# Kernel tuning notes

Hardware: AMD Instinct MI355X
Metric: run time of the kernel (lower is better)

Reference implementation:

```python
import jax, jax.numpy as jnp
import numpy as np

NUM_HEADS = 8
QK_CH = 1024
V_CH = 1024
Q_DIM = 1024
KV_DIM = 1024
EPS = 1e-5


def layernorm(x, w, b):
    mu = jnp.mean(x, axis=-1, keepdims=True)
    var = jnp.mean(jnp.square(x - mu), axis=-1, keepdims=True)
    return (x - mu) * jax.lax.rsqrt(var + EPS) * w + b


def setup_inputs() -> dict:
    key = jax.random.key(0)
    ks = jax.random.split(key, 8)
    B, Q, K = 8, 512, 4096
    s = 0.02
    return {
        "hidden_states": jax.random.normal(ks[0], (B, Q, Q_DIM), jnp.float32),
        "inputs": jax.random.normal(ks[1], (B, K, KV_DIM), jnp.float32),
        "ln1_w": jnp.ones((Q_DIM,), jnp.float32),
        "ln1_b": jnp.zeros((Q_DIM,), jnp.float32),
        "ln2_w": jnp.ones((KV_DIM,), jnp.float32),
        "ln2_b": jnp.zeros((KV_DIM,), jnp.float32),
        "Wq": jax.random.normal(ks[2], (QK_CH, Q_DIM), jnp.float32) * s,
        "bq": jnp.zeros((QK_CH,), jnp.float32),
        "Wk": jax.random.normal(ks[3], (QK_CH, KV_DIM), jnp.float32) * s,
        "bk": jnp.zeros((QK_CH,), jnp.float32),
        "Wv": jax.random.normal(ks[4], (V_CH, KV_DIM), jnp.float32) * s,
        "bv": jnp.zeros((V_CH,), jnp.float32),
    }


def reference(hidden_states, inputs, ln1_w, ln1_b, ln2_w, ln2_b, Wq, bq, Wk, bk, Wv, bv):
    B, Qlen, _ = hidden_states.shape
    Klen = inputs.shape[1]
    H = NUM_HEADS
    dqk = QK_CH // H
    dv = V_CH // H

    h = layernorm(hidden_states, ln1_w, ln1_b)
    x = layernorm(inputs, ln2_w, ln2_b)

    # torch Linear: y = x W^T + b
    q = (h @ Wq.T + bq).reshape(B, Qlen, H, dqk).transpose(0, 2, 1, 3)  # b h q d
    k = (x @ Wk.T + bk).reshape(B, Klen, H, dqk).transpose(0, 2, 1, 3)  # b h k d
    v = (x @ Wv.T + bv).reshape(B, Klen, H, dv).transpose(0, 2, 1, 3)   # b h k d

    scores = jnp.einsum("bhqd,bhkd->bhqk", q, k) / jnp.sqrt(jnp.float32(dqk))
    probs = jax.nn.softmax(scores, axis=-1)
    ctx = jnp.einsum("bhqk,bhkd->bhqd", probs, v)
    ctx = ctx.transpose(0, 2, 1, 3).reshape(B, Qlen, H * dv)

    # use_query_residual=True
    return hidden_states + ctx
```

## Files before the change

### kernel.cpp

```cpp
#include <hip/hip_runtime.h>
#include <hip/hip_fp8.h>

typedef __attribute__((ext_vector_type(8))) short short8;
typedef __attribute__((ext_vector_type(4))) short bf16x4;
typedef __attribute__((ext_vector_type(4))) float f32x4;
typedef __attribute__((ext_vector_type(2))) long i64x2;

#define DEV __device__ __forceinline__

DEV unsigned short f2bf(float f) {
    unsigned int u = __builtin_bit_cast(unsigned int, f);
    u += 0x7fffu + ((u >> 16) & 1u);
    return (unsigned short)(u >> 16);
}

DEV unsigned char f2fp8(float f) {
    return __hip_fp8_e4m3(f).__x;
}

#define GLOAD16(gp, lp)                                                        \
    __builtin_amdgcn_global_load_lds(                                          \
        (const __attribute__((address_space(1))) void*)(gp),                   \
        (__attribute__((address_space(3))) void*)(lp), 16, 0, 0)

__global__ __launch_bounds__(256) void prep(
    const float* __restrict__ hidden, const float* __restrict__ inputs,
    const float* __restrict__ ln1w, const float* __restrict__ ln1b,
    const float* __restrict__ ln2w, const float* __restrict__ ln2b,
    const float* __restrict__ Wq, const float* __restrict__ Wk, const float* __restrict__ Wv,
    unsigned char* __restrict__ LNh8, unsigned char* __restrict__ LNx8,
    unsigned char* __restrict__ Wq8, unsigned char* __restrict__ Wk8, unsigned char* __restrict__ Wv8)
{
    if (blockIdx.x < 9216) {
        int row = blockIdx.x * 4 + (threadIdx.x >> 6);
        int lane = threadIdx.x & 63;
        const float *src, *wp, *bp; unsigned char* dst;
        if (row < 4096) { src = hidden + (size_t)row * 1024; wp = ln1w; bp = ln1b; dst = LNh8 + (size_t)row * 1024; }
        else { int r = row - 4096; src = inputs + (size_t)r * 1024; wp = ln2w; bp = ln2b; dst = LNx8 + (size_t)r * 1024; }

        f32x4 v[4];
        float s = 0.f, ss = 0.f;
#pragma unroll
        for (int i = 0; i < 4; ++i) {
            v[i] = *reinterpret_cast<const f32x4*>(src + lane * 16 + i * 4);
#pragma unroll
            for (int j = 0; j < 4; ++j) { s += v[i][j]; ss += v[i][j] * v[i][j]; }
        }
#pragma unroll
        for (int off = 32; off >= 1; off >>= 1) { s += __shfl_xor(s, off); ss += __shfl_xor(ss, off); }
        float mu = s * (1.f / 1024.f);
        float var = fmaxf(ss * (1.f / 1024.f) - mu * mu, 0.f);
        float rs = rsqrtf(var + 1e-5f);

        unsigned char by[16];
#pragma unroll
        for (int i = 0; i < 4; ++i) {
            f32x4 wv = *reinterpret_cast<const f32x4*>(wp + lane * 16 + i * 4);
            f32x4 bv = *reinterpret_cast<const f32x4*>(bp + lane * 16 + i * 4);
#pragma unroll
            for (int j = 0; j < 4; ++j)
                by[i * 4 + j] = f2fp8((v[i][j] - mu) * rs * wv[j] + bv[j]);
        }
        int o = (lane * 16) & 63;
        int s0 = (o < 32) ? 2 * o : 2 * (o - 32) + 8;
        unsigned char* base = dst + (lane >> 2) * 64;
        *reinterpret_cast<unsigned long long*>(base + s0)      = *reinterpret_cast<unsigned long long*>(&by[0]);
        *reinterpret_cast<unsigned long long*>(base + s0 + 16) = *reinterpret_cast<unsigned long long*>(&by[8]);
    } else {
        unsigned tid = (blockIdx.x - 9216) * 256 + threadIdx.x;
        int arr = tid >> 16;
        unsigned idx = tid & 65535u;
        const float* s = (arr == 0) ? Wq : (arr == 1) ? Wk : Wv;
        unsigned char* d = (arr == 0) ? Wq8 : (arr == 1) ? Wk8 : Wv8;
        unsigned char by[16];
#pragma unroll
        for (int i = 0; i < 4; ++i) {
            f32x4 a = *reinterpret_cast<const f32x4*>(s + (size_t)idx * 16 + i * 4);
#pragma unroll
            for (int j = 0; j < 4; ++j) by[i * 4 + j] = f2fp8(a[j] * 64.f);
        }
        int o = (idx & 3) * 16;
        int s0 = (o < 32) ? 2 * o : 2 * (o - 32) + 8;
        unsigned char* base = d + (size_t)(idx >> 2) * 64;
        *reinterpret_cast<unsigned long long*>(base + s0)      = *reinterpret_cast<unsigned long long*>(&by[0]);
        *reinterpret_cast<unsigned long long*>(base + s0 + 16) = *reinterpret_cast<unsigned long long*>(&by[8]);
    }
}

__global__ __launch_bounds__(512, 2) void gemm256(
    const unsigned char* __restrict__ A8, const unsigned char* __restrict__ Ah8,
    const unsigned char* __restrict__ W8, const unsigned char* __restrict__ Wq8,
    const float* __restrict__ bk, const float* __restrict__ bv, const float* __restrict__ bq,
    unsigned short* __restrict__ Cn, unsigned short* __restrict__ Vt, unsigned short* __restrict__ Qm)
{
    __shared__ __align__(16) char smemc[65536];

    int t = threadIdx.x, lane = t & 63, w = t >> 6, g = lane >> 4, lr = lane & 15;
    int wr = w >> 2, wcn = w & 3;
    int R0 = wr * 128, C0 = wcn * 64;

    int id = blockIdx.x;
    int m0, n0, trans = 0;
    const unsigned char *Ab_, *Wb_;
    const float* bias;
    unsigned short* Cout;
    if (id < 1024) {
        int xcd = id & 7, ord = id >> 3;
        int mt = xcd * 16 + ord / 8;
        int nt = ord % 8;
        m0 = mt * 256; n0 = nt * 256;
        Ab_ = A8; Wb_ = W8;
        if (nt < 4) { bias = bk; Cout = Cn; }
        else        { bias = bv; Cout = Vt; trans = 1; }
    } else {
        int id2 = id - 1024;
        int mt = id2 & 15, nt = id2 >> 4;
        m0 = mt * 256; n0 = nt * 256;
        Ab_ = Ah8; Wb_ = Wq8;
        bias = bq; Cout = Qm;
    }

    const unsigned char* Ap = Ab_ + (size_t)m0 * 1024;
    const unsigned char* Wp = Wb_ + (size_t)n0 * 1024;

    f32x4 acc[8][4];
#pragma unroll
    for (int i = 0; i < 8; ++i)
#pragma unroll
        for (int j = 0; j < 4; ++j) acc[i][j] = (f32x4)0.f;

    int schunk = (t & 3) ^ ((t >> 3) & 3);
    auto STAGE1 = [&](int slot, int kt, int q) {
        const unsigned char* P = (q < 2) ? Ap : Wp;
        char* ldsb = smemc + ((q < 2) ? 0 : 32768) + slot * 16384 + (q & 1) * 8192;
        int r = (q & 1) * 128 + (t >> 2);
        const char* gp = (const char*)(P + (size_t)r * 1024 + kt * 64 + schunk * 16);
        GLOAD16(gp, ldsb + (t >> 2) * 64 + (t & 3) * 16);
    };

    STAGE1(0, 0, 0); STAGE1(0, 0, 1); STAGE1(0, 0, 2); STAGE1(0, 0, 3);
    asm volatile("s_waitcnt vmcnt(0)" ::: "memory");
    __builtin_amdgcn_s_barrier();

    int xr = (lr >> 1) & 3;
    int slA = (g ^ xr) * 16;

    for (int kt = 0; kt < 16; ++kt) {
        const int cs = kt & 1;
        const char* Ab = smemc + cs * 16384;
        const char* Bb = smemc + 32768 + cs * 16384;
        i64x2 af[4], bf[4];

#pragma unroll
        for (int a = 0; a < 4; ++a) {
            int r = R0 + a * 16 + lr;
            af[a] = *reinterpret_cast<const i64x2*>(Ab + r * 64 + slA);
        }
#pragma unroll
        for (int ni = 0; ni < 4; ++ni) {
            int r = C0 + ni * 16 + lr;
            bf[ni] = *reinterpret_cast<const i64x2*>(Bb + r * 64 + slA);
        }
        if (kt < 15) { STAGE1(cs ^ 1, kt + 1, 0); STAGE1(cs ^ 1, kt + 1, 1); }
        __builtin_amdgcn_sched_barrier(0);
        __builtin_amdgcn_s_barrier();
        asm volatile("s_waitcnt lgkmcnt(0)" ::: "memory");
        __builtin_amdgcn_sched_barrier(0);
        __builtin_amdgcn_s_setprio(1);
#pragma unroll
        for (int a = 0; a < 4; ++a)
#pragma unroll
            for (int ni = 0; ni < 4; ++ni) {
                acc[a][ni] = __builtin_amdgcn_mfma_f32_16x16x32_fp8_fp8(
                    af[a][0], bf[ni][0], acc[a][ni], 0, 0, 0);
                acc[a][ni] = __builtin_amdgcn_mfma_f32_16x16x32_fp8_fp8(
                    af[a][1], bf[ni][1], acc[a][ni], 0, 0, 0);
            }
        __builtin_amdgcn_s_setprio(0);
        __builtin_amdgcn_sched_barrier(0);
        __builtin_amdgcn_s_barrier();

#pragma unroll
        for (int a = 0; a < 4; ++a) {
            int r = R0 + 64 + a * 16 + lr;
            af[a] = *reinterpret_cast<const i64x2*>(Ab + r * 64 + slA);
        }
        if (kt < 15) { STAGE1(cs ^ 1, kt + 1, 2); STAGE1(cs ^ 1, kt + 1, 3); }
        __builtin_amdgcn_sched_barrier(0);
        __builtin_amdgcn_s_barrier();
        asm volatile("s_waitcnt lgkmcnt(0)" ::: "memory");
        __builtin_amdgcn_sched_barrier(0);
        __builtin_amdgcn_s_setprio(1);
#pragma unroll
        for (int a = 0; a < 4; ++a)
#pragma unroll
            for (int ni = 0; ni < 4; ++ni) {
                acc[4 + a][ni] = __builtin_amdgcn_mfma_f32_16x16x32_fp8_fp8(
                    af[a][0], bf[ni][0], acc[4 + a][ni], 0, 0, 0);
                acc[4 + a][ni] = __builtin_amdgcn_mfma_f32_16x16x32_fp8_fp8(
                    af[a][1], bf[ni][1], acc[4 + a][ni], 0, 0, 0);
            }
        __builtin_amdgcn_s_setprio(0);
        asm volatile("s_waitcnt vmcnt(0)" ::: "memory");
        __builtin_amdgcn_sched_barrier(0);
        __builtin_amdgcn_s_barrier();
    }
    __syncthreads();

    const float SC = 0.015625f;
    unsigned short* CtS = (unsigned short*)smemc;
    if (!trans) {
#pragma unroll
        for (int ch = 0; ch < 4; ++ch) {
            if (ch) __syncthreads();
            if (wr == (ch >> 1)) {
                int ma = (ch & 1) * 4;
#pragma unroll
                for (int ni = 0; ni < 4; ++ni) {
                    int c = C0 + ni * 16 + lr;
                    float bvv = bias[n0 + c];
#pragma unroll
                    for (int a = 0; a < 4; ++a)
#pragma unroll
                        for (int j = 0; j < 4; ++j)
                            CtS[(a * 16 + g * 4 + j) * 272 + c] = f2bf(acc[ma + a][ni][j] * SC + bvv);
                }
            }
            __syncthreads();
#pragma unroll
            for (int it = 0; it < 4; ++it) {
                int u2 = it * 512 + t;
                int row = u2 >> 5, c16 = u2 & 31;
                *reinterpret_cast<short8*>(Cout + (size_t)(m0 + ch * 64 + row) * 1024 + n0 + c16 * 8) =
                    *reinterpret_cast<const short8*>(&CtS[row * 272 + c16 * 8]);
            }
        }
    } else {
        int nt = n0 >> 8;
        int hbase = (nt - 4) * 2;
        int b = m0 >> 12, kv0 = m0 & 4095;
#pragma unroll
        for (int ch = 0; ch < 4; ++ch) {
            if (ch) __syncthreads();
            if (wcn == ch) {
#pragma unroll
                for (int ni = 0; ni < 4; ++ni) {
                    int dl = ni * 16 + lr;
                    float bvv = bias[(nt - 4) * 256 + ch * 64 + dl];
#pragma unroll
                    for (int mi = 0; mi < 8; ++mi)
#pragma unroll
                        for (int j = 0; j < 4; ++j)
                            CtS[dl * 272 + R0 + mi * 16 + g * 4 + j] = f2bf(acc[mi][ni][j] * SC + bvv);
                }
            }
            __syncthreads();
            int hh = hbase + (ch >> 1), dbase = (ch & 1) * 64;
            unsigned short* dst = Cout + ((size_t)(b * 8 + hh) * 128 + dbase) * 4096 + kv0;
#pragma unroll
            for (int it = 0; it < 4; ++it) {
                int u2 = it * 512 + t;
                int row = u2 >> 5, c8 = u2 & 31;
                *reinterpret_cast<short8*>(dst + (size_t)row * 4096 + c8 * 8) =
                    *reinterpret_cast<const short8*>(&CtS[row * 272 + c8 * 8]);
            }
        }
    }
}

__global__ __launch_bounds__(256, 2) void attn_kernel(
    const unsigned short* __restrict__ Qm, const unsigned short* __restrict__ Km,
    const unsigned short* __restrict__ VtG, const float* __restrict__ hidden,
    float* __restrict__ out)
{
    __shared__ __align__(16) unsigned short Kl[2][64 * 128];
    __shared__ __align__(16) unsigned short Vt[2][128 * 64];
    __shared__ __align__(16) unsigned short Pl[64 * 64];

    int t = threadIdx.x, lane = t & 63, w = t >> 6, g = lane >> 4, lr = lane & 15;
    int id = blockIdx.x;
    int swz = (id & 7) * 64 + (id >> 3);
    int qt = swz & 7, h = (swz >> 3) & 7, b = swz >> 6;

    short8 qf[4];
#pragma unroll
    for (int kk = 0; kk < 4; ++kk)
        qf[kk] = *reinterpret_cast<const short8*>(
            Qm + (size_t)(b * 512 + qt * 64 + w * 16 + lr) * 1024 + h * 128 + kk * 32 + g * 8);
    asm volatile("s_waitcnt vmcnt(0)" ::: "memory");

    float m2 = 0.f;
    float l = 0.f;
    f32x4 oacc[8];
#pragma unroll
    for (int nf = 0; nf < 8; ++nf) oacc[nf] = (f32x4)0.f;

    const float SCALE = 0.08838834764831845f;
    const float LOG2E = 1.4426950408889634f;
    const float K1 = SCALE * LOG2E;
    const float THR2 = 11.5f;

    size_t kbase = (size_t)b * 4096 * 1024 + h * 128;
    size_t vbase = ((size_t)(b * 8 + h)) * 128 * 4096;

    auto STAGE_K = [&](int buf, int c) {
        int kv0 = c * 64;
#pragma unroll
        for (int i = 0; i < 4; ++i) {
            int rb = w * 16 + i * 4;
            int row = rb + (lane >> 4);
            int cb = ((lane & 15) * 16) ^ ((row & 7) << 4);
            const char* gp = (const char*)(Km + kbase + (size_t)(kv0 + row) * 1024) + cb;
            GLOAD16(gp, &Kl[buf][rb * 128]);
        }
    };
    auto STAGE_V = [&](int buf, int c) {
        int kv0 = c * 64;
#pragma unroll
        for (int i = 0; i < 4; ++i) {
            int db = w * 32 + i * 8;
            int d = db + (lane >> 3);
            int cb = ((lane & 7) * 16) ^ ((d & 7) << 4);
            const char* gp = (const char*)(VtG + vbase + (size_t)d * 4096 + kv0) + cb;
            GLOAD16(gp, &Vt[buf][db * 64]);
        }
    };

    STAGE_K(0, 0); STAGE_V(0, 0);

    for (int c = 0; c < 64; ++c) {
        int cur = c & 1;
        asm volatile("s_waitcnt vmcnt(0) lgkmcnt(0)" ::: "memory");
        __builtin_amdgcn_sched_barrier(0);
        __builtin_amdgcn_s_barrier();
        if (c < 63) { STAGE_K(cur ^ 1, c + 1); STAGE_V(cur ^ 1, c + 1); }

        f32x4 sacc[4];
#pragma unroll
        for (int nf = 0; nf < 4; ++nf) sacc[nf] = (f32x4)0.f;
#pragma unroll
        for (int kk = 0; kk < 4; ++kk) {
            int cb0 = kk * 64 + g * 16;
            short8 kf[4];
#pragma unroll
            for (int nf = 0; nf < 4; ++nf) {
                int row = nf * 16 + lr;
                kf[nf] = *reinterpret_cast<const short8*>(
                    (const char*)&Kl[cur][0] + row * 256 + (cb0 ^ ((row & 7) << 4)));
            }
            __builtin_amdgcn_s_setprio(1);
#pragma unroll
            for (int nf = 0; nf < 4; ++nf)
                sacc[nf] = __builtin_amdgcn_mfma_f32_16x16x32_bf16(kf[nf], qf[kk], sacc[nf], 0, 0, 0);
            __builtin_amdgcn_s_setprio(0);
        }

        float smax = sacc[0][0];
#pragma unroll
        for (int nf = 0; nf < 4; ++nf)
#pragma unroll
            for (int j = 0; j < 4; ++j) smax = fmaxf(smax, sacc[nf][j]);
        float s2max = smax * K1;
        if (!__all(s2max <= m2 + THR2)) {
            float rm = s2max;
            rm = fmaxf(rm, __shfl_xor(rm, 16));
            rm = fmaxf(rm, __shfl_xor(rm, 32));
            float m2n = fmaxf(m2, rm);
            float corr = exp2f(m2 - m2n);
            l *= corr;
            m2 = m2n;
#pragma unroll
            for (int j = 0; j < 4; ++j) {
                float cj = __shfl(corr, g * 4 + j);
#pragma unroll
                for (int nf = 0; nf < 8; ++nf) oacc[nf][j] *= cj;
            }
        }
        int prow = w * 16 + lr;
        int rsw = (lr & 7) << 4;
#pragma unroll
        for (int nf = 0; nf < 4; ++nf) {
            float p0 = exp2f(sacc[nf][0] * K1 - m2);
            float p1 = exp2f(sacc[nf][1] * K1 - m2);
            float p2 = exp2f(sacc[nf][2] * K1 - m2);
            float p3 = exp2f(sacc[nf][3] * K1 - m2);
            l += (p0 + p1) + (p2 + p3);
            bf16x4 pk;
            pk[0] = (short)f2bf(p0); pk[1] = (short)f2bf(p1);
            pk[2] = (short)f2bf(p2); pk[3] = (short)f2bf(p3);
            *reinterpret_cast<bf16x4*>(
                (char*)Pl + prow * 128 + ((nf * 32 + g * 8) ^ rsw)) = pk;
        }
        asm volatile("s_waitcnt lgkmcnt(0)" ::: "memory");
        __builtin_amdgcn_sched_barrier(0);

#pragma unroll
        for (int kp = 0; kp < 2; ++kp) {
            int cb0 = kp * 64 + g * 16;
            short8 pa = *reinterpret_cast<const short8*>(
                (const char*)Pl + prow * 128 + (cb0 ^ rsw));
#pragma unroll
            for (int nf = 0; nf < 8; ++nf) {
                int d = nf * 16 + lr;
                short8 vb = *reinterpret_cast<const short8*>(
                    (const char*)&Vt[cur][0] + d * 128 + (cb0 ^ ((d & 7) << 4)));
                oacc[nf] = __builtin_amdgcn_mfma_f32_16x16x32_bf16(pa, vb, oacc[nf], 0, 0, 0);
            }
        }
    }

    l += __shfl_xor(l, 16);
    l += __shfl_xor(l, 32);
#pragma unroll
    for (int j = 0; j < 4; ++j) {
        float lj = __shfl(l, g * 4 + j);
        float inv = 1.f / lj;
        int q = qt * 64 + w * 16 + g * 4 + j;
        size_t base = (size_t)(b * 512 + q) * 1024 + h * 128;
#pragma unroll
        for (int nf = 0; nf < 8; ++nf) {
            int d = nf * 16 + lr;
            out[base + d] = hidden[base + d] + oacc[nf][j] * inv;
        }
    }
}

extern "C" void kernel_launch(void* const* d_in, const int* in_sizes, int n_in,
                              void* d_out, int out_size, void* d_ws, size_t ws_size,
                              hipStream_t stream) {
    const float* hidden = (const float*)d_in[0];
    const float* inputs = (const float*)d_in[1];
    const float* ln1w   = (const float*)d_in[2];
    const float* ln1b   = (const float*)d_in[3];
    const float* ln2w   = (const float*)d_in[4];
    const float* ln2b   = (const float*)d_in[5];
    const float* Wq     = (const float*)d_in[6];
    const float* bq     = (const float*)d_in[7];
    const float* Wk     = (const float*)d_in[8];
    const float* bk     = (const float*)d_in[9];
    const float* Wv     = (const float*)d_in[10];
    const float* bv     = (const float*)d_in[11];
    float* out = (float*)d_out;
    char* ws = (char*)d_ws;

    unsigned char* LNh8 = (unsigned char*)ws;
    unsigned char* LNx8 = LNh8 + 4194304;
    unsigned char* Wq8  = LNx8 + 33554432;
    unsigned char* Wk8  = Wq8 + 1048576;
    unsigned char* Wv8  = Wk8 + 1048576;
    unsigned short* Qm  = (unsigned short*)(Wv8 + 1048576);
    unsigned short* Km  = Qm + 4194304;
    unsigned short* VtG = Km + 33554432;

    prep<<<dim3(9984), dim3(256), 0, stream>>>(
        hidden, inputs, ln1w, ln1b, ln2w, ln2b, Wq, Wk, Wv, LNh8, LNx8, Wq8, Wk8, Wv8);
    gemm256<<<dim3(1088), dim3(512), 0, stream>>>(
        LNx8, LNh8, Wk8, Wq8, bk, bv, bq, Km, VtG, Qm);
    attn_kernel<<<dim3(512), dim3(256), 0, stream>>>(Qm, Km, VtG, hidden, out);
}
```

Before: 293.9 us.

## Store Q/K/V and attention probabilities in FP8 and use FP8 MFMA in attention

The projection GEMM now writes Q, K and transposed V as FP8 e4m3 instead of bf16, with a permuted column layout matching the fp8 MFMA operand order. The attention kernel stages half-size K/V tiles, computes QK^T and PV with fp8 MFMA, and packs probabilities to fp8 in LDS with new swizzles. The online-softmax rescale threshold is lowered to limit fp8 range issues on probabilities. This halves the intermediate memory traffic and LDS footprint and uses a higher-throughput MFMA, at the cost of precision in the scores and in the probability accumulation.

Measured after the change: 300.4 us. 1.02x slower.

```diff
diff --git a/kernel.cpp b/kernel.cpp
--- a/kernel.cpp
+++ b/kernel.cpp
@@ -22,6 +22,10 @@
     __builtin_amdgcn_global_load_lds(                                          \
         (const __attribute__((address_space(1))) void*)(gp),                   \
         (__attribute__((address_space(3))) void*)(lp), 16, 0, 0)
+
+DEV int pi64(int o) {
+    return (o < 32) ? ((o >> 3) * 16 + (o & 7)) : (((o - 32) >> 3) * 16 + 8 + (o & 7));
+}
 
 __global__ __launch_bounds__(256) void prep(
     const float* __restrict__ hidden, const float* __restrict__ inputs,
@@ -91,7 +95,7 @@
     const unsigned char* __restrict__ A8, const unsigned char* __restrict__ Ah8,
     const unsigned char* __restrict__ W8, const unsigned char* __restrict__ Wq8,
     const float* __restrict__ bk, const float* __restrict__ bv, const float* __restrict__ bq,
-    unsigned short* __restrict__ Cn, unsigned short* __restrict__ Vt, unsigned short* __restrict__ Qm)
+    unsigned char* __restrict__ Cn, unsigned char* __restrict__ Vt, unsigned char* __restrict__ Qm)
 {
     __shared__ __align__(16) char smemc[65536];
 
@@ -103,7 +107,7 @@
     int m0, n0, trans = 0;
     const unsigned char *Ab_, *Wb_;
     const float* bias;
-    unsigned short* Cout;
+    unsigned char* Cout;
     if (id < 1024) {
         int xcd = id & 7, ord = id >> 3;
         int mt = xcd * 16 + ord / 8;
@@ -208,7 +212,7 @@
     __syncthreads();
 
     const float SC = 0.015625f;
-    unsigned short* CtS = (unsigned short*)smemc;
+    unsigned char* CtS8 = (unsigned char*)smemc;
     if (!trans) {
 #pragma unroll
         for (int ch = 0; ch < 4; ++ch) {
@@ -219,20 +223,21 @@
                 for (int ni = 0; ni < 4; ++ni) {
                     int c = C0 + ni * 16 + lr;
                     float bvv = bias[n0 + c];
+                    int cc = (c & ~63) + pi64(c & 63);
 #pragma unroll
                     for (int a = 0; a < 4; ++a)
 #pragma unroll
                         for (int j = 0; j < 4; ++j)
-                            CtS[(a * 16 + g * 4 + j) * 272 + c] = f2bf(acc[ma + a][ni][j] * SC + bvv);
+                            CtS8[(a * 16 + g * 4 + j) * 272 + cc] = f2fp8(acc[ma + a][ni][j] * SC + bvv);
                 }
             }
             __syncthreads();
 #pragma unroll
-            for (int it = 0; it < 4; ++it) {
+            for (int it = 0; it < 2; ++it) {
                 int u2 = it * 512 + t;
-                int row = u2 >> 5, c16 = u2 & 31;
-                *reinterpret_cast<short8*>(Cout + (size_t)(m0 + ch * 64 + row) * 1024 + n0 + c16 * 8) =
-                    *reinterpret_cast<const short8*>(&CtS[row * 272 + c16 * 8]);
+                int row = u2 >> 4, c16 = u2 & 15;
+                *reinterpret_cast<f32x4*>(Cout + (size_t)(m0 + ch * 64 + row) * 1024 + n0 + c16 * 16) =
+                    *reinterpret_cast<const f32x4*>(&CtS8[row * 272 + c16 * 16]);
             }
         }
     } else {
@@ -251,42 +256,43 @@
                     for (int mi = 0; mi < 8; ++mi)
 #pragma unroll
                         for (int j = 0; j < 4; ++j)
-                            CtS[dl * 272 + R0 + mi * 16 + g * 4 + j] = f2bf(acc[mi][ni][j] * SC + bvv);
+                            CtS8[dl * 272 + R0 + mi * 16 + g * 4 + j] = f2fp8(acc[mi][ni][j] * SC + bvv);
                 }
             }
             __syncthreads();
             int hh = hbase + (ch >> 1), dbase = (ch & 1) * 64;
-            unsigned short* dst = Cout + ((size_t)(b * 8 + hh) * 128 + dbase) * 4096 + kv0;
-#pragma unroll
-            for (int it = 0; it < 4; ++it) {
+            unsigned char* dst = Cout + ((size_t)(b * 8 + hh) * 128 + dbase) * 4096 + kv0;
+#pragma unroll
+            for (int it = 0; it < 2; ++it) {
                 int u2 = it * 512 + t;
-                int row = u2 >> 5, c8 = u2 & 31;
-                *reinterpret_cast<short8*>(dst + (size_t)row * 4096 + c8 * 8) =
-                    *reinterpret_cast<const short8*>(&CtS[row * 272 + c8 * 8]);
+                int row = u2 >> 4, c16 = u2 & 15;
+                *reinterpret_cast<f32x4*>(dst + (size_t)row * 4096 + c16 * 16) =
+                    *reinterpret_cast<const f32x4*>(&CtS8[row * 272 + c16 * 16]);
             }
         }
     }
 }
 
 __global__ __launch_bounds__(256, 2) void attn_kernel(
-    const unsigned short* __restrict__ Qm, const unsigned short* __restrict__ Km,
-    const unsigned short* __restrict__ VtG, const float* __restrict__ hidden,
+    const unsigned char* __restrict__ Qm8, const unsigned char* __restrict__ Km8,
+    const unsigned char* __restrict__ Vt8, const float* __restrict__ hidden,
     float* __restrict__ out)
 {
-    __shared__ __align__(16) unsigned short Kl[2][64 * 128];
-    __shared__ __align__(16) unsigned short Vt[2][128 * 64];
-    __shared__ __align__(16) unsigned short Pl[64 * 64];
+    __shared__ __align__(16) unsigned char Kl[2][64 * 128];
+    __shared__ __align__(16) unsigned char Vt[2][128 * 64];
+    __shared__ __align__(16) unsigned char Pl[64 * 64];
 
     int t = threadIdx.x, lane = t & 63, w = t >> 6, g = lane >> 4, lr = lane & 15;
     int id = blockIdx.x;
     int swz = (id & 7) * 64 + (id >> 3);
     int qt = swz & 7, h = (swz >> 3) & 7, b = swz >> 6;
 
-    short8 qf[4];
-#pragma unroll
-    for (int kk = 0; kk < 4; ++kk)
-        qf[kk] = *reinterpret_cast<const short8*>(
-            Qm + (size_t)(b * 512 + qt * 64 + w * 16 + lr) * 1024 + h * 128 + kk * 32 + g * 8);
+    i64x2 qf[2];
+    {
+        const unsigned char* qp = Qm8 + (size_t)(b * 512 + qt * 64 + w * 16 + lr) * 1024 + h * 128;
+        qf[0] = *reinterpret_cast<const i64x2*>(qp + g * 16);
+        qf[1] = *reinterpret_cast<const i64x2*>(qp + 64 + g * 16);
+    }
     asm volatile("s_waitcnt vmcnt(0)" ::: "memory");
 
     float m2 = 0.f;
@@ -298,7 +304,7 @@
     const float SCALE = 0.08838834764831845f;
     const float LOG2E = 1.4426950408889634f;
     const float K1 = SCALE * LOG2E;
-    const float THR2 = 11.5f;
+    const float THR2 = 8.0f;
 
     size_t kbase = (size_t)b * 4096 * 1024 + h * 128;
     size_t vbase = ((size_t)(b * 8 + h)) * 128 * 4096;
@@ -306,27 +312,29 @@
     auto STAGE_K = [&](int buf, int c) {
         int kv0 = c * 64;
 #pragma unroll
-        for (int i = 0; i < 4; ++i) {
-            int rb = w * 16 + i * 4;
-            int row = rb + (lane >> 4);
-            int cb = ((lane & 15) * 16) ^ ((row & 7) << 4);
-            const char* gp = (const char*)(Km + kbase + (size_t)(kv0 + row) * 1024) + cb;
+        for (int i = 0; i < 2; ++i) {
+            int rb = w * 16 + i * 8;
+            int row = rb + (lane >> 3);
+            int cb = ((lane & 7) ^ (row & 7)) * 16;
+            const unsigned char* gp = Km8 + kbase + (size_t)(kv0 + row) * 1024 + cb;
             GLOAD16(gp, &Kl[buf][rb * 128]);
         }
     };
     auto STAGE_V = [&](int buf, int c) {
         int kv0 = c * 64;
 #pragma unroll
-        for (int i = 0; i < 4; ++i) {
-            int db = w * 32 + i * 8;
-            int d = db + (lane >> 3);
-            int cb = ((lane & 7) * 16) ^ ((d & 7) << 4);
-            const char* gp = (const char*)(VtG + vbase + (size_t)d * 4096 + kv0) + cb;
+        for (int i = 0; i < 2; ++i) {
+            int db = w * 32 + i * 16;
+            int d = db + (lane >> 2);
+            int cb = ((lane & 3) ^ ((d >> 1) & 3)) * 16;
+            const unsigned char* gp = Vt8 + vbase + (size_t)d * 4096 + kv0 + cb;
             GLOAD16(gp, &Vt[buf][db * 64]);
         }
     };
 
     STAGE_K(0, 0); STAGE_V(0, 0);
+
+    int rsw8 = (lr & 7) << 3;
 
     for (int c = 0; c < 64; ++c) {
         int cur = c & 1;
@@ -339,19 +347,20 @@
 #pragma unroll
         for (int nf = 0; nf < 4; ++nf) sacc[nf] = (f32x4)0.f;
 #pragma unroll
-        for (int kk = 0; kk < 4; ++kk) {
-            int cb0 = kk * 64 + g * 16;
-            short8 kf[4];
+        for (int kk2 = 0; kk2 < 2; ++kk2) {
+            i64x2 kf[4];
 #pragma unroll
             for (int nf = 0; nf < 4; ++nf) {
                 int row = nf * 16 + lr;
-                kf[nf] = *reinterpret_cast<const short8*>(
-                    (const char*)&Kl[cur][0] + row * 256 + (cb0 ^ ((row & 7) << 4)));
+                kf[nf] = *reinterpret_cast<const i64x2*>(
+                    &Kl[cur][row * 128 + ((kk2 * 64 + g * 16) ^ ((row & 7) << 4))]);
             }
             __builtin_amdgcn_s_setprio(1);
 #pragma unroll
-            for (int nf = 0; nf < 4; ++nf)
-                sacc[nf] = __builtin_amdgcn_mfma_f32_16x16x32_bf16(kf[nf], qf[kk], sacc[nf], 0, 0, 0);
+            for (int nf = 0; nf < 4; ++nf) {
+                sacc[nf] = __builtin_amdgcn_mfma_f32_16x16x32_fp8_fp8(kf[nf][0], qf[kk2][0], sacc[nf], 0, 0, 0);
+                sacc[nf] = __builtin_amdgcn_mfma_f32_16x16x32_fp8_fp8(kf[nf][1], qf[kk2][1], sacc[nf], 0, 0, 0);
+            }
             __builtin_amdgcn_s_setprio(0);
         }
 
@@ -377,7 +386,6 @@
             }
         }
         int prow = w * 16 + lr;
-        int rsw = (lr & 7) << 4;
 #pragma unroll
         for (int nf = 0; nf < 4; ++nf) {
             float p0 = exp2f(sacc[nf][0] * K1 - m2);
@@ -385,26 +393,25 @@
             float p2 = exp2f(sacc[nf][2] * K1 - m2);
             float p3 = exp2f(sacc[nf][3] * K1 - m2);
             l += (p0 + p1) + (p2 + p3);
-            bf16x4 pk;
-            pk[0] = (short)f2bf(p0); pk[1] = (short)f2bf(p1);
-            pk[2] = (short)f2bf(p2); pk[3] = (short)f2bf(p3);
-            *reinterpret_cast<bf16x4*>(
-                (char*)Pl + prow * 128 + ((nf * 32 + g * 8) ^ rsw)) = pk;
+            unsigned pk = (unsigned)f2fp8(p0) | ((unsigned)f2fp8(p1) << 8) |
+                          ((unsigned)f2fp8(p2) << 16) | ((unsigned)f2fp8(p3) << 24);
+            int pos = nf * 16 + g * 4;
+            *reinterpret_cast<unsigned*>(
+                &Pl[prow * 64 + ((pos & 0x38) ^ rsw8) + (pos & 7)]) = pk;
         }
         asm volatile("s_waitcnt lgkmcnt(0)" ::: "memory");
         __builtin_amdgcn_sched_barrier(0);
 
 #pragma unroll
         for (int kp = 0; kp < 2; ++kp) {
-            int cb0 = kp * 64 + g * 16;
-            short8 pa = *reinterpret_cast<const short8*>(
-                (const char*)Pl + prow * 128 + (cb0 ^ rsw));
+            long pa = *reinterpret_cast<const long*>(
+                &Pl[prow * 64 + ((kp * 32 + g * 8) ^ rsw8)]);
 #pragma unroll
             for (int nf = 0; nf < 8; ++nf) {
                 int d = nf * 16 + lr;
-                short8 vb = *reinterpret_cast<const short8*>(
-                    (const char*)&Vt[cur][0] + d * 128 + (cb0 ^ ((d & 7) << 4)));
-                oacc[nf] = __builtin_amdgcn_mfma_f32_16x16x32_bf16(pa, vb, oacc[nf], 0, 0, 0);
+                long vb = *reinterpret_cast<const long*>(
+                    &Vt[cur][d * 64 + ((kp * 32 + g * 8) ^ ((d & 6) << 3))]);
+                oacc[nf] = __builtin_amdgcn_mfma_f32_16x16x32_fp8_fp8(pa, vb, oacc[nf], 0, 0, 0);
             }
         }
     }
@@ -448,13 +455,13 @@
     unsigned char* Wq8  = LNx8 + 33554432;
     unsigned char* Wk8  = Wq8 + 1048576;
     unsigned char* Wv8  = Wk8 + 1048576;
-    unsigned short* Qm  = (unsigned short*)(Wv8 + 1048576);
-    unsigned short* Km  = Qm + 4194304;
-    unsigned short* VtG = Km + 33554432;
+    unsigned char* Qm8  = Wv8 + 1048576;
+    unsigned char* Km8  = Qm8 + 4194304;
+    unsigned char* Vt8  = Km8 + 33554432;
 
     prep<<<dim3(9984), dim3(256), 0, stream>>>(
         hidden, inputs, ln1w, ln1b, ln2w, ln2b, Wq, Wk, Wv, LNh8, LNx8, Wq8, Wk8, Wv8);
     gemm256<<<dim3(1088), dim3(512), 0, stream>>>(
-        LNx8, LNh8, Wk8, Wq8, bk, bv, bq, Km, VtG, Qm);
-    attn_kernel<<<dim3(512), dim3(256), 0, stream>>>(Qm, Km, VtG, hidden, out);
-}
+        LNx8, LNh8, Wk8, Wq8, bk, bv, bq, Km8, Vt8, Qm8);
+    attn_kernel<<<dim3(512), dim3(256), 0, stream>>>(Qm8, Km8, Vt8, hidden, out);
+}
```
